# Optimization experiments

Hardware: AMD Instinct MI355X
Metric: run time of the kernel (lower is better)

## Reference

```python
import jax, jax.numpy as jnp
import numpy as np

L, B, T, C, H, D, F, W = 2, 2, 2048, 1024, 16, 64, 4096, 256
NEG = -1e9
EPS = 1e-6


def _rms(x, g):
    return x * jax.lax.rsqrt(jnp.mean(x * x, axis=-1, keepdims=True) + EPS) * g


def setup_inputs() -> dict:
    key = jax.random.key(0)
    ks = jax.random.split(key, 12)
    s = 0.02
    return {
        "x": jax.random.normal(ks[0], (B, T, C), jnp.float32),
        "retrieval_context": jax.random.normal(ks[1], (B, C), jnp.float32),
        "norm1_g": jnp.ones((L, C), jnp.float32),
        "Wqkv": jax.random.normal(ks[2], (L, C, 3 * C), jnp.float32) * s,
        "Wproj": jax.random.normal(ks[3], (L, C, C), jnp.float32) * s,
        "gate_W": jax.random.normal(ks[4], (L, C, 3), jnp.float32) * 0.01,
        "gate_b": jnp.zeros((L, 3), jnp.float32),
        "ret_W": jax.random.normal(ks[5], (L, C, C), jnp.float32) * 0.01,
        "norm2_g": jnp.ones((L, C), jnp.float32),
        "ffn_gate_W": jax.random.normal(ks[6], (L, C, F), jnp.float32) * s,
        "ffn_up_W": jax.random.normal(ks[7], (L, C, F), jnp.float32) * s,
        "ffn_down_W": jax.random.normal(ks[8], (L, F, C), jnp.float32) * s,
    }


def reference(x, retrieval_context, norm1_g, Wqkv, Wproj, gate_W, gate_b, ret_W,
              norm2_g, ffn_gate_W, ffn_up_W, ffn_down_W):
    # Sliding-window causal mask: key j visible to query i iff i-W+1 <= j <= i
    pos = jnp.arange(T)
    allowed = (pos[None, :] <= pos[:, None]) & (pos[None, :] >= pos[:, None] - W + 1)
    mask = jnp.where(allowed, 0.0, NEG).astype(x.dtype)  # (T, T)
    scale = 1.0 / np.sqrt(D)

    for l in range(L):
        h = _rms(x, norm1_g[l])                              # (B,T,C)
        qkv = h @ Wqkv[l]                                    # (B,T,3C)
        q, k, v = jnp.split(qkv, 3, axis=-1)
        q = q.reshape(B, T, H, D).transpose(0, 2, 1, 3)       # (B,H,T,D)
        k = k.reshape(B, T, H, D).transpose(0, 2, 1, 3)
        v = v.reshape(B, T, H, D).transpose(0, 2, 1, 3)
        scores = jnp.einsum("bhqd,bhkd->bhqk", q, k) * scale + mask
        attn = jax.nn.softmax(scores, axis=-1)
        o = jnp.einsum("bhqk,bhkd->bhqd", attn, v)
        attn_out = o.transpose(0, 2, 1, 3).reshape(B, T, C) @ Wproj[l]

        # TRN disabled: trn_out == 0, gate channel 1 pinned to -1e9
        gate_logits = h @ gate_W[l] + gate_b[l]               # (B,T,3)
        gate_logits = gate_logits.at[..., 1].set(NEG)
        gates = jax.nn.softmax(gate_logits, axis=-1)

        ret_out = (retrieval_context @ ret_W[l])[:, None, :]   # (B,1,C) broadcast over T
        mixed = gates[..., 0:1] * attn_out + gates[..., 2:3] * ret_out
        x = x + mixed

        h2 = _rms(x, norm2_g[l])
        ffn = (jax.nn.silu(h2 @ ffn_gate_W[l]) * (h2 @ ffn_up_W[l])) @ ffn_down_W[l]
        x = x + ffn
    return x
```

## Files before the change

### kernel.cpp

```cpp
#include <hip/hip_runtime.h>

#define L_ 2
#define B_ 2
#define T_ 2048
#define C_ 1024
#define H_ 16
#define D_ 64
#define F_ 4096
#define NTOK 4096
#define NELEM 4194304

typedef unsigned short u16;
typedef __attribute__((ext_vector_type(8))) short short8;
typedef __attribute__((ext_vector_type(4))) float float4v;

__device__ __forceinline__ float bf2f(u16 u) {
  unsigned v = ((unsigned)u) << 16;
  return __builtin_bit_cast(float, v);
}
__device__ __forceinline__ u16 f2bf(float f) {
  unsigned u = __builtin_bit_cast(unsigned, f);
  u += 0x7FFFu + ((u >> 16) & 1u);
  return (u16)(u >> 16);
}

__device__ __forceinline__ void xcd_swz(int& bx, int& by) {
  const int gy4 = gridDim.y >> 2;
  const int f = by * 16 + bx;
  const int k = f & 7, s = f >> 3;
  bx = ((k & 1) << 3) + (s & 7);
  by = (k >> 1) * gy4 + (s >> 3);
}

__global__ void k_copyf_acc(const float* __restrict__ in, float* __restrict__ out) {
  const int i = blockIdx.x * 256 + threadIdx.x;
  out[i] = in[i] + out[i];
}

__device__ __forceinline__ void rms_gate_tail(float* vloc, const float* __restrict__ g,
                                              u16* __restrict__ orow,
                                              const float* __restrict__ gw3,
                                              const float* __restrict__ gb3,
                                              float* __restrict__ gates, int row) {
  float s = vloc[0] * vloc[0] + vloc[1] * vloc[1] + vloc[2] * vloc[2] + vloc[3] * vloc[3];
#pragma unroll
  for (int o = 32; o; o >>= 1) s += __shfl_down(s, o);
  __shared__ float red[4];
  __shared__ float rsv;
  if ((threadIdx.x & 63) == 0) red[threadIdx.x >> 6] = s;
  __syncthreads();
  if (threadIdx.x == 0) {
    float t = red[0] + red[1] + red[2] + red[3];
    rsv = rsqrtf(t * (1.f / C_) + 1e-6f);
  }
  __syncthreads();
  const float rr = rsv;
  float s0 = 0.f, s2 = 0.f;
#pragma unroll
  for (int i = 0; i < 4; i++) {
    const int c = threadIdx.x + i * 256;
    const float h = vloc[i] * rr * g[c];
    orow[c] = f2bf(h);
    s0 += h * gw3[c * 3 + 0];
    s2 += h * gw3[c * 3 + 2];
  }
#pragma unroll
  for (int o = 32; o; o >>= 1) { s0 += __shfl_down(s0, o); s2 += __shfl_down(s2, o); }
  __shared__ float r0[4], r2[4];
  if ((threadIdx.x & 63) == 0) { r0[threadIdx.x >> 6] = s0; r2[threadIdx.x >> 6] = s2; }
  __syncthreads();
  if (threadIdx.x == 0) {
    const float l0 = r0[0] + r0[1] + r0[2] + r0[3] + gb3[0];
    const float l2 = r2[0] + r2[1] + r2[2] + r2[3] + gb3[2];
    const float m = fmaxf(l0, l2);
    const float e0 = __expf(l0 - m), e2 = __expf(l2 - m);
    const float inv = 1.f / (e0 + e2);
    gates[row * 2 + 0] = e0 * inv;
    gates[row * 2 + 1] = e2 * inv;
  }
}

__global__ __launch_bounds__(256) void k_rms_first(const float* __restrict__ xin,
                                                   const float* __restrict__ g,
                                                   float* __restrict__ x,
                                                   u16* __restrict__ out,
                                                   const float* __restrict__ gw3,
                                                   const float* __restrict__ gb3,
                                                   float* __restrict__ gates) {
  const int row = blockIdx.x;
  const float* sr = xin + (size_t)row * C_;
  float* xr = x + (size_t)row * C_;
  float vloc[4];
#pragma unroll
  for (int i = 0; i < 4; i++) {
    const int c = threadIdx.x + i * 256;
    const float v = sr[c];
    vloc[i] = v;
    xr[c] = v;
  }
  rms_gate_tail(vloc, g, out + (size_t)row * C_, gw3, gb3, gates, row);
}

__global__ __launch_bounds__(256) void k_rms_acc(float* __restrict__ x,
                                                 const float* __restrict__ pf,
                                                 const float* __restrict__ g,
                                                 u16* __restrict__ out,
                                                 const float* __restrict__ gw3,
                                                 const float* __restrict__ gb3,
                                                 float* __restrict__ gates) {
  const int row = blockIdx.x;
  float* xr = x + (size_t)row * C_;
  const float* pr = pf + (size_t)row * C_;
  float vloc[4];
#pragma unroll
  for (int i = 0; i < 4; i++) {
    const int c = threadIdx.x + i * 256;
    const float v = xr[c] + pr[c];
    vloc[i] = v;
    xr[c] = v;
  }
  rms_gate_tail(vloc, g, out + (size_t)row * C_, gw3, gb3, gates, row);
}

__global__ __launch_bounds__(256) void k_rms2mix(float* __restrict__ x,
                                                 const float* __restrict__ gates,
                                                 const float* __restrict__ ret,
                                                 const float* __restrict__ pf,
                                                 const float* __restrict__ g,
                                                 u16* __restrict__ out) {
  const int row = blockIdx.x;
  const int b = row >> 11;
  const float g2 = gates[row * 2 + 1];
  const float* rr_ = ret + b * C_;
  const float* pr = pf + (size_t)row * C_;
  float* xr = x + (size_t)row * C_;
  float vloc[4];
#pragma unroll
  for (int i = 0; i < 4; i++) {
    const int c = threadIdx.x + i * 256;
    const float v = xr[c] + pr[c] + g2 * rr_[c];
    vloc[i] = v;
    xr[c] = v;
  }
  float s = vloc[0] * vloc[0] + vloc[1] * vloc[1] + vloc[2] * vloc[2] + vloc[3] * vloc[3];
#pragma unroll
  for (int o = 32; o; o >>= 1) s += __shfl_down(s, o);
  __shared__ float red[4];
  __shared__ float rsv;
  if ((threadIdx.x & 63) == 0) red[threadIdx.x >> 6] = s;
  __syncthreads();
  if (threadIdx.x == 0) {
    float t = red[0] + red[1] + red[2] + red[3];
    rsv = rsqrtf(t * (1.f / C_) + 1e-6f);
  }
  __syncthreads();
  const float rr = rsv;
  u16* orow = out + (size_t)row * C_;
#pragma unroll
  for (int i = 0; i < 4; i++) {
    const int c = threadIdx.x + i * 256;
    orow[c] = f2bf(vloc[i] * rr * g[c]);
  }
}

__global__ void k_tr2(const float* __restrict__ s0, u16* __restrict__ d0,
                      int K0, int N0, int t0,
                      const float* __restrict__ s1, u16* __restrict__ d1,
                      int K1, int N1) {
  __shared__ float tile[32][33];
  int t = blockIdx.x;
  const float* src; u16* dst; int K, N;
  if (t < t0) { src = s0; dst = d0; K = K0; N = N0; }
  else { t -= t0; src = s1; dst = d1; K = K1; N = N1; }
  const int ntx = N >> 5;
  const int tx = t % ntx, ty = t / ntx;
  const int x = tx * 32 + threadIdx.x;
  const int y0 = ty * 32 + threadIdx.y;
#pragma unroll
  for (int i = 0; i < 32; i += 8) tile[threadIdx.y + i][threadIdx.x] = src[(size_t)(y0 + i) * N + x];
  __syncthreads();
  const int x2 = ty * 32 + threadIdx.x;
  const int y2 = tx * 32 + threadIdx.y;
#pragma unroll
  for (int i = 0; i < 32; i += 8) dst[(size_t)(y2 + i) * K + x2] = f2bf(tile[threadIdx.x][threadIdx.y + i]);
}

__global__ void k_tr1(const float* __restrict__ in, u16* __restrict__ out, int K, int N) {
  __shared__ float tile[32][33];
  const int ntx = N >> 5;
  const int tx = blockIdx.x % ntx, ty = blockIdx.x / ntx;
  const int x = tx * 32 + threadIdx.x;
  const int y0 = ty * 32 + threadIdx.y;
#pragma unroll
  for (int i = 0; i < 32; i += 8) tile[threadIdx.y + i][threadIdx.x] = in[(size_t)(y0 + i) * N + x];
  __syncthreads();
  const int x2 = ty * 32 + threadIdx.x;
  const int y2 = tx * 32 + threadIdx.y;
#pragma unroll
  for (int i = 0; i < 32; i += 8) out[(size_t)(y2 + i) * K + x2] = f2bf(tile[threadIdx.x][threadIdx.y + i]);
}

__global__ void k_vt(const u16* __restrict__ qkv, u16* __restrict__ Vt) {
  __shared__ u16 tile[32][34];
  const int jt = blockIdx.x;
  const int dt = blockIdx.y;
  const int bh = blockIdx.z;
  const int b = bh >> 4;
  const int h = bh & 15;
  const int tx = threadIdx.x, ty = threadIdx.y;
#pragma unroll
  for (int i = 0; i < 32; i += 8) {
    const int j = jt * 32 + ty + i;
    const int d = dt * 32 + tx;
    tile[ty + i][tx] = qkv[(size_t)(b * T_ + j) * (3 * C_) + 2 * C_ + h * D_ + d];
  }
  __syncthreads();
#pragma unroll
  for (int i = 0; i < 32; i += 8) {
    const int d = dt * 32 + ty + i;
    const int j = jt * 32 + tx;
    Vt[(size_t)(bh * D_ + d) * T_ + j] = tile[tx][ty + i];
  }
}

#define VMW(n) asm volatile("s_waitcnt vmcnt(" #n ")" ::: "memory")
#define LGKM0 asm volatile("s_waitcnt lgkmcnt(0)" ::: "memory")
#define GBAR() __builtin_amdgcn_s_barrier()
#define PRIO1() __builtin_amdgcn_s_setprio(1)
#define PRIO0() __builtin_amdgcn_s_setprio(0)

#define STG8(gsrc, grow0, dstbyte, kk)                                                    \
  do {                                                                                    \
    const u16* g0_ = (gsrc) + (size_t)((grow0) + wid * 8 + srow) * K + (kk) + scol;       \
    __builtin_amdgcn_global_load_lds(                                                     \
        (const __attribute__((address_space(1))) void*)g0_,                               \
        (__attribute__((address_space(3))) void*)(lc + (dstbyte) + wid * 8 * 128),        \
        16, 0, 0);                                                                        \
    const u16* g1_ = g0_ + (size_t)64 * K;                                                \
    __builtin_amdgcn_global_load_lds(                                                     \
        (const __attribute__((address_space(1))) void*)g1_,                               \
        (__attribute__((address_space(3))) void*)(lc + (dstbyte) + (64 + wid * 8) * 128), \
        16, 0, 0);                                                                        \
  } while (0)

#define RDA4(dst, bufbyte, ig0)                                                           \
  { _Pragma("unroll") for (int i_ = 0; i_ < 4; ++i_) {                                    \
      _Pragma("unroll") for (int s_ = 0; s_ < 2; ++s_)                                    \
        dst[i_][s_] = *(const short8*)(lc + (bufbyte) +                                   \
            (wm * 128 + ((ig0) + i_) * 16 + m16) * 128 + (((s_ * 4 + quad) ^ csw) * 16)); } }

#define RDB4(dst, bufbyte, jg0)                                                           \
  { _Pragma("unroll") for (int j_ = 0; j_ < 2; ++j_) {                                    \
      _Pragma("unroll") for (int s_ = 0; s_ < 2; ++s_)                                    \
        dst[j_][s_] = *(const short8*)(lc + (bufbyte) +                                   \
            (wn * 64 + ((jg0) + j_) * 16 + m16) * 128 + (((s_ * 4 + quad) ^ csw) * 16)); } }

#define RDBS(dst, bufbyte)                                                                \
  { _Pragma("unroll") for (int j_ = 0; j_ < 2; ++j_) {                                    \
      _Pragma("unroll") for (int s_ = 0; s_ < 2; ++s_)                                    \
        dst[j_][s_] = *(const short8*)(lc + (bufbyte) +                                   \
            (wn * 32 + j_ * 16 + m16) * 128 + (((s_ * 4 + quad) ^ csw) * 16)); } }

#define MM16(ig0, jg0, bv_)                                                               \
  { _Pragma("unroll") for (int i_ = 0; i_ < 4; ++i_) {                                    \
      _Pragma("unroll") for (int j_ = 0; j_ < 2; ++j_) {                                  \
        _Pragma("unroll") for (int s_ = 0; s_ < 2; ++s_)                                  \
          acc[(ig0) + i_][(jg0) + j_] = __builtin_amdgcn_mfma_f32_16x16x32_bf16(          \
              av[i_][s_], bv_[j_][s_], acc[(ig0) + i_][(jg0) + j_], 0, 0, 0); } } }

#define MMS(accv, ig0, bv_)                                                               \
  { _Pragma("unroll") for (int i_ = 0; i_ < 4; ++i_) {                                    \
      _Pragma("unroll") for (int j_ = 0; j_ < 2; ++j_) {                                  \
        _Pragma("unroll") for (int s_ = 0; s_ < 2; ++s_)                                  \
          accv[(ig0) + i_][j_] = __builtin_amdgcn_mfma_f32_16x16x32_bf16(                 \
              av[i_][s_], bv_[j_][s_], accv[(ig0) + i_][j_], 0, 0, 0); } } }

#define MMN(ig0, bv_)                                                                     \
  { _Pragma("unroll") for (int i_ = 0; i_ < 4; ++i_) {                                    \
      _Pragma("unroll") for (int j_ = 0; j_ < 2; ++j_) {                                  \
        _Pragma("unroll") for (int s_ = 0; s_ < 2; ++s_)                                  \
          acc[(ig0) + i_][j_] = __builtin_amdgcn_mfma_f32_16x16x32_bf16(                  \
              av8[(ig0) + i_][s_], bv_[j_][s_], acc[(ig0) + i_][j_], 0, 0, 0); } } }

__global__ __launch_bounds__(512, 2) void k_g256(const u16* __restrict__ A,
                                                 const u16* __restrict__ Bt,
                                                 u16* __restrict__ Cc,
                                                 int N, int K) {
  extern __shared__ __align__(16) u16 lds[];
  char* const lc = (char*)lds;
  enum { A0B = 0, B0B = 32768, A1B = 65536, B1B = 98304 };
  const int tid = threadIdx.x;
  const int wid = tid >> 6, lane = tid & 63;
  const int wm = wid >> 2, wn = wid & 3;
  const int quad = lane >> 4, m16 = lane & 15;
  const int srow = lane >> 3, sc = lane & 7;
  const int scol = ((sc ^ srow) & 7) * 8;
  const int csw = m16 & 7;
  int bx = blockIdx.x, by = blockIdx.y;
  xcd_swz(bx, by);
  const int m0 = bx * 256, n0 = by * 256;
  const int kbeg = 0;
  const int ntile = K >> 6;
  const int nit = ntile >> 1;

  float4v acc[8][4];
#pragma unroll
  for (int i = 0; i < 8; i++)
#pragma unroll
    for (int j = 0; j < 4; j++) acc[i][j] = (float4v){0.f, 0.f, 0.f, 0.f};
  short8 av[4][2], b01[2][2], b23[2][2];

  STG8(Bt, n0, B0B, kbeg);
  STG8(Bt, n0 + 128, B0B + 16384, kbeg);
  STG8(A, m0, A0B, kbeg);
  STG8(A, m0 + 128, A0B + 16384, kbeg);
  STG8(Bt, n0, B1B, kbeg + 64);
  STG8(Bt, n0 + 128, B1B + 16384, kbeg + 64);
  VMW(4);
  GBAR();

#pragma unroll 1
  for (int it = 0; it < nit; ++it) {
    const int t2 = 2 * it + 2, t3 = 2 * it + 3;
    const int k1 = kbeg + (2 * it + 1) * 64;
    const int k2 = kbeg + (t2 < ntile ? t2 : t2 - ntile) * 64;
    const int k3 = kbeg + (t3 < ntile ? t3 : t3 - ntile) * 64;
    RDA4(av, A0B, 0);
    RDB4(b01, B0B, 0);
    STG8(A, m0, A1B, k1);
    GBAR(); LGKM0;
    PRIO1(); MM16(0, 0, b01); PRIO0();
    GBAR();
    RDB4(b23, B0B, 2);
    STG8(A, m0 + 128, A1B + 16384, k1);
    GBAR(); LGKM0;
    PRIO1(); MM16(0, 2, b23); PRIO0();
    GBAR();
    RDA4(av, A0B, 4);
    STG8(Bt, n0, B0B, k2);
    GBAR(); LGKM0;
    PRIO1(); MM16(4, 2, b23); PRIO0();
    GBAR();
    STG8(Bt, n0 + 128, B0B + 16384, k2);
    VMW(4);
    GBAR(); LGKM0;
    PRIO1(); MM16(4, 0, b01); PRIO0();
    GBAR();
    RDA4(av, A1B, 0);
    RDB4(b01, B1B, 0);
    STG8(A, m0, A0B, k2);
    GBAR(); LGKM0;
    PRIO1(); MM16(0, 0, b01); PRIO0();
    GBAR();
    RDB4(b23, B1B, 2);
    STG8(A, m0 + 128, A0B + 16384, k2);
    GBAR(); LGKM0;
    PRIO1(); MM16(0, 2, b23); PRIO0();
    GBAR();
    RDA4(av, A1B, 4);
    STG8(Bt, n0, B1B, k3);
    GBAR(); LGKM0;
    PRIO1(); MM16(4, 2, b23); PRIO0();
    GBAR();
    STG8(Bt, n0 + 128, B1B + 16384, k3);
    VMW(4);
    GBAR(); LGKM0;
    PRIO1(); MM16(4, 0, b01); PRIO0();
    GBAR();
  }

#pragma unroll
  for (int i = 0; i < 8; i++) {
    const int row0 = m0 + wm * 128 + i * 16 + quad * 4;
#pragma unroll
    for (int j = 0; j < 4; j++) {
      const int col = n0 + wn * 64 + j * 16 + m16;
#pragma unroll
      for (int r = 0; r < 4; r++)
        Cc[(size_t)(row0 + r) * N + col] = f2bf(acc[i][j][r]);
    }
  }
}

template <int EPI>
__global__ __launch_bounds__(512, 2) void k_g256n(const u16* __restrict__ A,
                                                  const u16* __restrict__ Bt,
                                                  float* __restrict__ Xf,
                                                  float* __restrict__ Pf,
                                                  const float* __restrict__ gates,
                                                  int N, int K) {
  extern __shared__ __align__(16) u16 lds[];
  char* const lc = (char*)lds;
  enum { SA0 = 0, SB0 = 32768, SA1 = 49152, SB1 = 81920 };
  const int tid = threadIdx.x;
  const int wid = tid >> 6, lane = tid & 63;
  const int wm = wid >> 2, wn = wid & 3;
  const int quad = lane >> 4, m16 = lane & 15;
  const int srow = lane >> 3, sc = lane & 7;
  const int scol = ((sc ^ srow) & 7) * 8;
  const int csw = m16 & 7;
  int bx = blockIdx.x, by = blockIdx.y;
  xcd_swz(bx, by);
  const int m0 = bx * 256, n0 = by * 128;
  const int Kslice = K / gridDim.z;
  const int kbeg = blockIdx.z * Kslice;
  const int ntile = Kslice >> 6;
  const int nit = ntile >> 1;

  float4v acc[8][2];
#pragma unroll
  for (int i = 0; i < 8; i++)
#pragma unroll
    for (int j = 0; j < 2; j++) acc[i][j] = (float4v){0.f, 0.f, 0.f, 0.f};
  short8 av8[8][2], bv[2][2];

  STG8(Bt, n0, SB0, kbeg);
  STG8(A, m0, SA0, kbeg);
  STG8(A, m0 + 128, SA0 + 16384, kbeg);
  STG8(Bt, n0, SB1, kbeg + 64);
  STG8(A, m0, SA1, kbeg + 64);
  STG8(A, m0 + 128, SA1 + 16384, kbeg + 64);
  VMW(6);
  GBAR();

#pragma unroll 1
  for (int it = 0; it < nit; ++it) {
    const int t2 = 2 * it + 2, t3 = 2 * it + 3;
    const int k2 = kbeg + (t2 < ntile ? t2 : t2 - ntile) * 64;
    const int k3 = kbeg + (t3 < ntile ? t3 : t3 - ntile) * 64;
    RDA4(av8, SA0, 0);
    RDA4((&av8[4]), SA0, 4);
    RDBS(bv, SB0);
    GBAR(); LGKM0;
    PRIO1(); MMN(0, bv); PRIO0();
    GBAR();
    STG8(Bt, n0, SB0, k2);
    STG8(A, m0, SA0, k2);
    STG8(A, m0 + 128, SA0 + 16384, k2);
    VMW(6);
    GBAR(); LGKM0;
    PRIO1(); MMN(4, bv); PRIO0();
    GBAR();
    RDA4(av8, SA1, 0);
    RDA4((&av8[4]), SA1, 4);
    RDBS(bv, SB1);
    GBAR(); LGKM0;
    PRIO1(); MMN(0, bv); PRIO0();
    GBAR();
    STG8(Bt, n0, SB1, k3);
    STG8(A, m0, SA1, k3);
    STG8(A, m0 + 128, SA1 + 16384, k3);
    VMW(6);
    GBAR(); LGKM0;
    PRIO1(); MMN(4, bv); PRIO0();
    GBAR();
  }

#pragma unroll
  for (int i = 0; i < 8; i++) {
    const int row0 = m0 + wm * 128 + i * 16 + quad * 4;
#pragma unroll
    for (int j = 0; j < 2; j++) {
      const int col = n0 + wn * 32 + j * 16 + m16;
#pragma unroll
      for (int r = 0; r < 4; r++) {
        const size_t idx = (size_t)(row0 + r) * N + col;
        const float v = acc[i][j][r];
        const float sv = (EPI == 1) ? gates[(row0 + r) * 2] * v : v;
        if (blockIdx.z == 0) Pf[idx] = sv;
        else Xf[idx] += sv;
      }
    }
  }
}

__global__ __launch_bounds__(512, 2) void k_g256s(const u16* __restrict__ A,
                                                  const u16* __restrict__ Btg,
                                                  const u16* __restrict__ Btu,
                                                  u16* __restrict__ Cc,
                                                  int N, int K) {
  extern __shared__ __align__(16) u16 lds[];
  char* const lc = (char*)lds;
  enum { SA0 = 0, SG0 = 32768, SU0 = 49152, SA1 = 65536, SG1 = 98304, SU1 = 114688 };
  const int tid = threadIdx.x;
  const int wid = tid >> 6, lane = tid & 63;
  const int wm = wid >> 2, wn = wid & 3;
  const int quad = lane >> 4, m16 = lane & 15;
  const int srow = lane >> 3, sc = lane & 7;
  const int scol = ((sc ^ srow) & 7) * 8;
  const int csw = m16 & 7;
  int bx = blockIdx.x, by = blockIdx.y;
  xcd_swz(bx, by);
  const int m0 = bx * 256, n0 = by * 128;
  const int kbeg = 0;
  const int ntile = K >> 6;
  const int nit = ntile >> 1;

  float4v accg[8][2], accu[8][2];
#pragma unroll
  for (int i = 0; i < 8; i++)
#pragma unroll
    for (int j = 0; j < 2; j++) {
      accg[i][j] = (float4v){0.f, 0.f, 0.f, 0.f};
      accu[i][j] = (float4v){0.f, 0.f, 0.f, 0.f};
    }
  short8 av[4][2], bg[2][2], bu[2][2];

  STG8(Btg, n0, SG0, kbeg);
  STG8(Btu, n0, SU0, kbeg);
  STG8(A, m0, SA0, kbeg);
  STG8(A, m0 + 128, SA0 + 16384, kbeg);
  STG8(Btg, n0, SG1, kbeg + 64);
  STG8(Btu, n0, SU1, kbeg + 64);
  STG8(A, m0, SA1, kbeg + 64);
  VMW(6);
  GBAR();

#pragma unroll 1
  for (int it = 0; it < nit; ++it) {
    const int t2 = 2 * it + 2, t3 = 2 * it + 3;
    const int k1 = kbeg + (2 * it + 1) * 64;
    const int k2 = kbeg + (t2 < ntile ? t2 : t2 - ntile) * 64;
    const int k3 = kbeg + (t3 < ntile ? t3 : t3 - ntile) * 64;
    RDA4(av, SA0, 0);
    RDBS(bg, SG0);
    STG8(A, m0 + 128, SA1 + 16384, k1);
    GBAR(); LGKM0;
    PRIO1(); MMS(accg, 0, bg); PRIO0();
    GBAR();
    RDBS(bu, SU0);
    STG8(Btg, n0, SG0, k2);
    GBAR(); LGKM0;
    PRIO1(); MMS(accu, 0, bu); PRIO0();
    GBAR();
    RDA4(av, SA0, 4);
    STG8(Btu, n0, SU0, k2);
    GBAR(); LGKM0;
    PRIO1(); MMS(accu, 4, bu); PRIO0();
    GBAR();
    STG8(A, m0, SA0, k2);
    VMW(6);
    GBAR(); LGKM0;
    PRIO1(); MMS(accg, 4, bg); PRIO0();
    GBAR();
    RDA4(av, SA1, 0);
    RDBS(bg, SG1);
    STG8(A, m0 + 128, SA0 + 16384, k2);
    GBAR(); LGKM0;
    PRIO1(); MMS(accg, 0, bg); PRIO0();
    GBAR();
    RDBS(bu, SU1);
    STG8(Btg, n0, SG1, k3);
    GBAR(); LGKM0;
    PRIO1(); MMS(accu, 0, bu); PRIO0();
    GBAR();
    RDA4(av, SA1, 4);
    STG8(Btu, n0, SU1, k3);
    GBAR(); LGKM0;
    PRIO1(); MMS(accu, 4, bu); PRIO0();
    GBAR();
    STG8(A, m0, SA1, k3);
    VMW(6);
    GBAR(); LGKM0;
    PRIO1(); MMS(accg, 4, bg); PRIO0();
    GBAR();
  }

#pragma unroll
  for (int i = 0; i < 8; i++) {
    const int row0 = m0 + wm * 128 + i * 16 + quad * 4;
#pragma unroll
    for (int j = 0; j < 2; j++) {
      const int col = n0 + wn * 32 + j * 16 + m16;
#pragma unroll
      for (int r = 0; r < 4; r++) {
        const float g = accg[i][j][r];
        const float u = accu[i][j][r];
        Cc[(size_t)(row0 + r) * N + col] = f2bf(u * g / (1.f + __expf(-g)));
      }
    }
  }
}

__global__ __launch_bounds__(256) void k_attn(const u16* __restrict__ qkv,
                                              const u16* __restrict__ Vt,
                                              u16* __restrict__ o) {
  __shared__ u16 lds[4][16][290];
  const int wave = threadIdx.x >> 6;
  const int bid = ((blockIdx.x & 7) << 7) + (blockIdx.x >> 3);
  const int widG = bid * 4 + wave;
  const int lane = threadIdx.x & 63;
  const int quad = lane >> 4;
  const int c16 = lane & 15;
  const int qt = (widG & 127) * 16;
  const int h = (widG >> 7) & 15;
  const int b = widG >> 11;
  const size_t rs = 3 * C_;
  const int jt0 = qt - 256;

  const u16* qrow = qkv + (size_t)(b * T_ + qt + c16) * rs + h * D_ + quad * 8;
  const short8 a0 = *(const short8*)(qrow);
  const short8 a1 = *(const short8*)(qrow + 32);
  float4v S[17];
  const short8 z8 = (short8){0, 0, 0, 0, 0, 0, 0, 0};
#pragma unroll
  for (int t = 0; t < 17; t++) {
    if (jt0 + t * 16 + 15 < 0) { S[t] = (float4v){0.f, 0.f, 0.f, 0.f}; continue; }
    const int j = jt0 + t * 16 + c16;
    short8 b0 = z8, b1 = z8;
    if (j >= 0) {
      const u16* krow = qkv + (size_t)(b * T_ + j) * rs + C_ + h * D_ + quad * 8;
      b0 = *(const short8*)(krow);
      b1 = *(const short8*)(krow + 32);
    }
    float4v z = (float4v){0.f, 0.f, 0.f, 0.f};
    PRIO1();
    z = __builtin_amdgcn_mfma_f32_16x16x32_bf16(a0, b0, z, 0, 0, 0);
    z = __builtin_amdgcn_mfma_f32_16x16x32_bf16(a1, b1, z, 0, 0, 0);
    PRIO0();
    S[t] = z;
  }
#pragma unroll
  for (int r = 0; r < 4; r++) {
    const int q = qt + quad * 4 + r;
    float mx = -1.0e30f;
#pragma unroll
    for (int t = 0; t < 17; t++) {
      const int j = jt0 + t * 16 + c16;
      const int w = j - q + 255;
      const bool vis = (j >= 0) && (w >= 0) && (w < 256);
      if (vis) {
        const float s = S[t][r] * 0.125f;
        S[t][r] = s;
        mx = fmaxf(mx, s);
      } else {
        S[t][r] = -1.0e30f;
      }
    }
#pragma unroll
    for (int o2 = 1; o2 < 16; o2 <<= 1) mx = fmaxf(mx, __shfl_xor(mx, o2));
    float sum = 0.f;
#pragma unroll
    for (int t = 0; t < 17; t++) {
      const float e = (S[t][r] > -0.9e30f) ? __expf(S[t][r] - mx) : 0.f;
      S[t][r] = e;
      sum += e;
    }
#pragma unroll
    for (int o2 = 1; o2 < 16; o2 <<= 1) sum += __shfl_xor(sum, o2);
    const float inv = 1.f / fmaxf(sum, 1e-30f);
    const int prow = quad * 4 + r;
#pragma unroll
    for (int t = 0; t < 17; t++) lds[wave][prow][t * 16 + c16] = f2bf(S[t][r] * inv);
    lds[wave][prow][272 + c16] = 0;
  }
  __syncthreads();

  float4v acc[4];
#pragma unroll
  for (int md = 0; md < 4; md++) acc[md] = (float4v){0.f, 0.f, 0.f, 0.f};
  const u16* vtb = Vt + (size_t)((b * H_ + h) * D_) * T_;
  const uint* prow32 = (const uint*)(&lds[wave][c16][0]);
  union { short8 s8; uint u[4]; } bf;
#pragma unroll
  for (int c = 0; c < 9; c++) {
    const int jbase = jt0 + c * 32;
    if (jbase + 31 < 0) continue;
#pragma unroll
    for (int w2 = 0; w2 < 4; w2++) bf.u[w2] = prow32[c * 16 + quad * 4 + w2];
    int j0 = jbase + quad * 8;
    j0 = (j0 < 0) ? 0 : ((j0 > T_ - 8) ? (T_ - 8) : j0);
    PRIO1();
#pragma unroll
    for (int md = 0; md < 4; md++) {
      const short8 af = *(const short8*)(vtb + (size_t)(md * 16 + c16) * T_ + j0);
      acc[md] = __builtin_amdgcn_mfma_f32_16x16x32_bf16(af, bf.s8, acc[md], 0, 0, 0);
    }
    PRIO0();
  }
#pragma unroll
  for (int md = 0; md < 4; md++) {
    uint u0 = (uint)f2bf(acc[md][0]) | ((uint)f2bf(acc[md][1]) << 16);
    uint u1 = (uint)f2bf(acc[md][2]) | ((uint)f2bf(acc[md][3]) << 16);
    uint2 pk = make_uint2(u0, u1);
    u16* dst = o + (size_t)(b * T_ + qt + c16) * C_ + h * D_ + md * 16 + quad * 4;
    *(uint2*)dst = pk;
  }
}

__global__ void k_ret2(const float* __restrict__ rc, const float* __restrict__ rW,
                       float* __restrict__ ret) {
  const int l = blockIdx.x >> 3;
  const int bid = blockIdx.x & 7;
  const int b = bid >> 2;
  const int col = (bid & 3) * 256 + threadIdx.x;
  const float* rWl = rW + (size_t)l * C_ * C_;
  float s = 0.f;
  for (int k = 0; k < C_; k++) s += rc[b * C_ + k] * rWl[(size_t)k * C_ + col];
  ret[(size_t)l * B_ * C_ + b * C_ + col] = s;
}

extern "C" void kernel_launch(void* const* d_in, const int* in_sizes, int n_in,
                              void* d_out, int out_size, void* d_ws, size_t ws_size,
                              hipStream_t stream) {
  (void)in_sizes; (void)n_in; (void)out_size; (void)ws_size;
  const float* xin  = (const float*)d_in[0];
  const float* rc   = (const float*)d_in[1];
  const float* n1g  = (const float*)d_in[2];
  const float* Wqkv = (const float*)d_in[3];
  const float* Wpro = (const float*)d_in[4];
  const float* gW   = (const float*)d_in[5];
  const float* gb   = (const float*)d_in[6];
  const float* rW   = (const float*)d_in[7];
  const float* n2g  = (const float*)d_in[8];
  const float* fgW  = (const float*)d_in[9];
  const float* fuW  = (const float*)d_in[10];
  const float* fdW  = (const float*)d_in[11];

  static bool attr_done = false;
  if (!attr_done) {
    hipFuncSetAttribute((const void*)k_g256, hipFuncAttributeMaxDynamicSharedMemorySize, 131072);
    hipFuncSetAttribute((const void*)k_g256s, hipFuncAttributeMaxDynamicSharedMemorySize, 131072);
    hipFuncSetAttribute((const void*)k_g256n<1>, hipFuncAttributeMaxDynamicSharedMemorySize, 98304);
    hipFuncSetAttribute((const void*)k_g256n<2>, hipFuncAttributeMaxDynamicSharedMemorySize, 98304);
    attr_done = true;
  }

  char* w = (char*)d_ws;
  float* gates = (float*)(w);
  float* retb  = (float*)(w + 32768);
  float* xf32  = (float*)(w + 65536);
  u16* hbuf    = (u16*)(w + 65536 + (size_t)NELEM * 4);
  u16* big     = hbuf + NELEM;
  u16* qkv  = big;
  u16* obuf = big + (size_t)NTOK * 3 * C_;
  u16* gbuf = big;
  u16* wT  = (u16*)d_out;
  u16* wTp = wT + (size_t)3 * C_ * C_;
  u16* Vt  = (u16*)d_out + (size_t)NELEM;
  u16* wT2 = Vt;
  float* Pf  = (float*)d_out;
  float* Pf2 = (float*)big;

  k_ret2<<<16, 256, 0, stream>>>(rc, rW, retb);

  for (int l = 0; l < L_; l++) {
    if (l == 0)
      k_rms_first<<<NTOK, 256, 0, stream>>>(xin, n1g, xf32, hbuf,
                                            gW, gb, gates);
    else
      k_rms_acc<<<NTOK, 256, 0, stream>>>(xf32, Pf, n1g + l * C_, hbuf,
                                          gW + (size_t)l * C_ * 3, gb + l * 3, gates);
    k_tr2<<<3072 + 1024, dim3(32, 8), 0, stream>>>(
        Wqkv + (size_t)l * C_ * 3 * C_, wT, C_, 3 * C_, 3072,
        Wpro + (size_t)l * C_ * C_, wTp, C_, C_);
    k_g256<<<dim3(NTOK / 256, 3 * C_ / 256, 1), 512, 131072, stream>>>(
        hbuf, wT, qkv, 3 * C_, C_);
    k_vt<<<dim3(64, 2, 32), dim3(32, 8), 0, stream>>>(qkv, Vt);
    k_attn<<<1024, 256, 0, stream>>>(qkv, Vt, obuf);
    k_g256n<1><<<dim3(NTOK / 256, C_ / 128, 2), 512, 98304, stream>>>(
        obuf, wTp, xf32, Pf2, gates, C_, C_);
    k_rms2mix<<<NTOK, 256, 0, stream>>>(xf32, gates, retb + (size_t)l * B_ * C_,
                                        Pf2, n2g + l * C_, hbuf);
    k_tr2<<<4096 + 4096, dim3(32, 8), 0, stream>>>(
        fgW + (size_t)l * C_ * F_, wT, C_, F_, 4096,
        fuW + (size_t)l * C_ * F_, wT2, C_, F_);
    k_g256s<<<dim3(NTOK / 256, F_ / 128, 1), 512, 131072, stream>>>(
        hbuf, wT, wT2, gbuf, F_, C_);
    k_tr1<<<4096, dim3(32, 8), 0, stream>>>(fdW + (size_t)l * F_ * C_, hbuf, F_, C_);
    k_g256n<2><<<dim3(NTOK / 256, C_ / 128, 2), 512, 98304, stream>>>(
        gbuf, hbuf, xf32, Pf, nullptr, C_, F_);
  }

  k_copyf_acc<<<NELEM / 256, 256, 0, stream>>>(xf32, (float*)d_out);
}
```

Measured before the change: 786.5 us.

## Fuse V-transpose into QKV GEMM epilogue and unify SwiGLU GEMM via interleaved weights

The QKV GEMM epilogue now writes the V columns directly in transposed (b,h,d,t) layout, which removes the separate k_vt transpose kernel. The FFN gate and up weights are transposed into one interleaved matrix (16-row groups alternating gate/up), so the generic 256x256 GEMM computes both and applies SiLU*up in its epilogue, replacing the specialised k_g256s kernel. The retrieval projection kernel is also re-split across 256 blocks with a shared-memory K reduction for more parallelism. The trade-off is strided 8-byte Vt stores in the epilogue and a branch per column group.

New measurement: 746.2 us. 5.1% less time.

```diff
diff --git a/kernel.cpp b/kernel.cpp
--- a/kernel.cpp
+++ b/kernel.cpp
@@ -185,6 +185,31 @@
   for (int i = 0; i < 32; i += 8) dst[(size_t)(y2 + i) * K + x2] = f2bf(tile[threadIdx.x][threadIdx.y + i]);
 }
 
+__global__ void k_tr2i(const float* __restrict__ s0, const float* __restrict__ s1,
+                       u16* __restrict__ dst, int t0) {
+  __shared__ float tile[32][33];
+  int t = blockIdx.x;
+  const float* src; int ofs;
+  if (t < t0) { src = s0; ofs = 0; }
+  else { t -= t0; src = s1; ofs = 16; }
+  const int N = F_, K = C_;
+  const int ntx = N >> 5;
+  const int tx = t % ntx, ty = t / ntx;
+  const int x = tx * 32 + threadIdx.x;
+  const int y0 = ty * 32 + threadIdx.y;
+#pragma unroll
+  for (int i = 0; i < 32; i += 8) tile[threadIdx.y + i][threadIdx.x] = src[(size_t)(y0 + i) * N + x];
+  __syncthreads();
+  const int x2 = ty * 32 + threadIdx.x;
+  const int y2 = tx * 32 + threadIdx.y;
+#pragma unroll
+  for (int i = 0; i < 32; i += 8) {
+    const int n = y2 + i;
+    const int rowp = ((n >> 4) << 5) + (n & 15) + ofs;
+    dst[(size_t)rowp * K + x2] = f2bf(tile[threadIdx.x][threadIdx.y + i]);
+  }
+}
+
 __global__ void k_tr1(const float* __restrict__ in, u16* __restrict__ out, int K, int N) {
   __shared__ float tile[32][33];
   const int ntx = N >> 5;
@@ -198,29 +223,6 @@
   const int y2 = tx * 32 + threadIdx.y;
 #pragma unroll
   for (int i = 0; i < 32; i += 8) out[(size_t)(y2 + i) * K + x2] = f2bf(tile[threadIdx.x][threadIdx.y + i]);
-}
-
-__global__ void k_vt(const u16* __restrict__ qkv, u16* __restrict__ Vt) {
-  __shared__ u16 tile[32][34];
-  const int jt = blockIdx.x;
-  const int dt = blockIdx.y;
-  const int bh = blockIdx.z;
-  const int b = bh >> 4;
-  const int h = bh & 15;
-  const int tx = threadIdx.x, ty = threadIdx.y;
-#pragma unroll
-  for (int i = 0; i < 32; i += 8) {
-    const int j = jt * 32 + ty + i;
-    const int d = dt * 32 + tx;
-    tile[ty + i][tx] = qkv[(size_t)(b * T_ + j) * (3 * C_) + 2 * C_ + h * D_ + d];
-  }
-  __syncthreads();
-#pragma unroll
-  for (int i = 0; i < 32; i += 8) {
-    const int d = dt * 32 + ty + i;
-    const int j = jt * 32 + tx;
-    Vt[(size_t)(bh * D_ + d) * T_ + j] = tile[tx][ty + i];
-  }
 }
 
 #define VMW(n) asm volatile("s_waitcnt vmcnt(" #n ")" ::: "memory")
@@ -268,13 +270,6 @@
           acc[(ig0) + i_][(jg0) + j_] = __builtin_amdgcn_mfma_f32_16x16x32_bf16(          \
               av[i_][s_], bv_[j_][s_], acc[(ig0) + i_][(jg0) + j_], 0, 0, 0); } } }
 
-#define MMS(accv, ig0, bv_)                                                               \
-  { _Pragma("unroll") for (int i_ = 0; i_ < 4; ++i_) {                                    \
-      _Pragma("unroll") for (int j_ = 0; j_ < 2; ++j_) {                                  \
-        _Pragma("unroll") for (int s_ = 0; s_ < 2; ++s_)                                  \
-          accv[(ig0) + i_][j_] = __builtin_amdgcn_mfma_f32_16x16x32_bf16(                 \
-              av[i_][s_], bv_[j_][s_], accv[(ig0) + i_][j_], 0, 0, 0); } } }
-
 #define MMN(ig0, bv_)                                                                     \
   { _Pragma("unroll") for (int i_ = 0; i_ < 4; ++i_) {                                    \
       _Pragma("unroll") for (int j_ = 0; j_ < 2; ++j_) {                                  \
@@ -282,9 +277,11 @@
           acc[(ig0) + i_][j_] = __builtin_amdgcn_mfma_f32_16x16x32_bf16(                  \
               av8[(ig0) + i_][s_], bv_[j_][s_], acc[(ig0) + i_][j_], 0, 0, 0); } } }
 
+template <int EPI>
 __global__ __launch_bounds__(512, 2) void k_g256(const u16* __restrict__ A,
                                                  const u16* __restrict__ Bt,
                                                  u16* __restrict__ Cc,
+                                                 u16* __restrict__ Vt,
                                                  int N, int K) {
   extern __shared__ __align__(16) u16 lds[];
   char* const lc = (char*)lds;
@@ -369,15 +366,44 @@
     GBAR();
   }
 
-#pragma unroll
-  for (int i = 0; i < 8; i++) {
-    const int row0 = m0 + wm * 128 + i * 16 + quad * 4;
-#pragma unroll
-    for (int j = 0; j < 4; j++) {
-      const int col = n0 + wn * 64 + j * 16 + m16;
-#pragma unroll
-      for (int r = 0; r < 4; r++)
-        Cc[(size_t)(row0 + r) * N + col] = f2bf(acc[i][j][r]);
+  if (EPI == 3) {
+#pragma unroll
+    for (int i = 0; i < 8; i++) {
+      const int row0 = m0 + wm * 128 + i * 16 + quad * 4;
+#pragma unroll
+      for (int jp = 0; jp < 2; jp++) {
+        const int col = by * 128 + wn * 32 + jp * 16 + m16;
+#pragma unroll
+        for (int r = 0; r < 4; r++) {
+          const float g = acc[i][jp * 2][r];
+          const float u = acc[i][jp * 2 + 1][r];
+          Cc[(size_t)(row0 + r) * N + col] = f2bf(u * g / (1.f + __expf(-g)));
+        }
+      }
+    }
+  } else {
+#pragma unroll
+    for (int i = 0; i < 8; i++) {
+      const int row0 = m0 + wm * 128 + i * 16 + quad * 4;
+#pragma unroll
+      for (int j = 0; j < 4; j++) {
+        const int colb = n0 + wn * 64 + j * 16;
+        if (colb >= 2 * C_) {
+          const int d = colb + m16 - 2 * C_;
+          const int bh = d >> 6;
+          const int dd = d & 63;
+          const int b_ = row0 >> 11;
+          const int tok = row0 & (T_ - 1);
+          uint u0 = (uint)f2bf(acc[i][j][0]) | ((uint)f2bf(acc[i][j][1]) << 16);
+          uint u1 = (uint)f2bf(acc[i][j][2]) | ((uint)f2bf(acc[i][j][3]) << 16);
+          *(uint2*)(Vt + (size_t)((b_ * H_ + bh) * D_ + dd) * T_ + tok) = make_uint2(u0, u1);
+        } else {
+          const int col = colb + m16;
+#pragma unroll
+          for (int r = 0; r < 4; r++)
+            Cc[(size_t)(row0 + r) * N + col] = f2bf(acc[i][j][r]);
+        }
+      }
     }
   }
 }
@@ -474,114 +500,6 @@
   }
 }
 
-__global__ __launch_bounds__(512, 2) void k_g256s(const u16* __restrict__ A,
-                                                  const u16* __restrict__ Btg,
-                                                  const u16* __restrict__ Btu,
-                                                  u16* __restrict__ Cc,
-                                                  int N, int K) {
-  extern __shared__ __align__(16) u16 lds[];
-  char* const lc = (char*)lds;
-  enum { SA0 = 0, SG0 = 32768, SU0 = 49152, SA1 = 65536, SG1 = 98304, SU1 = 114688 };
-  const int tid = threadIdx.x;
-  const int wid = tid >> 6, lane = tid & 63;
-  const int wm = wid >> 2, wn = wid & 3;
-  const int quad = lane >> 4, m16 = lane & 15;
-  const int srow = lane >> 3, sc = lane & 7;
-  const int scol = ((sc ^ srow) & 7) * 8;
-  const int csw = m16 & 7;
-  int bx = blockIdx.x, by = blockIdx.y;
-  xcd_swz(bx, by);
-  const int m0 = bx * 256, n0 = by * 128;
-  const int kbeg = 0;
-  const int ntile = K >> 6;
-  const int nit = ntile >> 1;
-
-  float4v accg[8][2], accu[8][2];
-#pragma unroll
-  for (int i = 0; i < 8; i++)
-#pragma unroll
-    for (int j = 0; j < 2; j++) {
-      accg[i][j] = (float4v){0.f, 0.f, 0.f, 0.f};
-      accu[i][j] = (float4v){0.f, 0.f, 0.f, 0.f};
-    }
-  short8 av[4][2], bg[2][2], bu[2][2];
-
-  STG8(Btg, n0, SG0, kbeg);
-  STG8(Btu, n0, SU0, kbeg);
-  STG8(A, m0, SA0, kbeg);
-  STG8(A, m0 + 128, SA0 + 16384, kbeg);
-  STG8(Btg, n0, SG1, kbeg + 64);
-  STG8(Btu, n0, SU1, kbeg + 64);
-  STG8(A, m0, SA1, kbeg + 64);
-  VMW(6);
-  GBAR();
-
-#pragma unroll 1
-  for (int it = 0; it < nit; ++it) {
-    const int t2 = 2 * it + 2, t3 = 2 * it + 3;
-    const int k1 = kbeg + (2 * it + 1) * 64;
-    const int k2 = kbeg + (t2 < ntile ? t2 : t2 - ntile) * 64;
-    const int k3 = kbeg + (t3 < ntile ? t3 : t3 - ntile) * 64;
-    RDA4(av, SA0, 0);
-    RDBS(bg, SG0);
-    STG8(A, m0 + 128, SA1 + 16384, k1);
-    GBAR(); LGKM0;
-    PRIO1(); MMS(accg, 0, bg); PRIO0();
-    GBAR();
-    RDBS(bu, SU0);
-    STG8(Btg, n0, SG0, k2);
-    GBAR(); LGKM0;
-    PRIO1(); MMS(accu, 0, bu); PRIO0();
-    GBAR();
-    RDA4(av, SA0, 4);
-    STG8(Btu, n0, SU0, k2);
-    GBAR(); LGKM0;
-    PRIO1(); MMS(accu, 4, bu); PRIO0();
-    GBAR();
-    STG8(A, m0, SA0, k2);
-    VMW(6);
-    GBAR(); LGKM0;
-    PRIO1(); MMS(accg, 4, bg); PRIO0();
-    GBAR();
-    RDA4(av, SA1, 0);
-    RDBS(bg, SG1);
-    STG8(A, m0 + 128, SA0 + 16384, k2);
-    GBAR(); LGKM0;
-    PRIO1(); MMS(accg, 0, bg); PRIO0();
-    GBAR();
-    RDBS(bu, SU1);
-    STG8(Btg, n0, SG1, k3);
-    GBAR(); LGKM0;
-    PRIO1(); MMS(accu, 0, bu); PRIO0();
-    GBAR();
-    RDA4(av, SA1, 4);
-    STG8(Btu, n0, SU1, k3);
-    GBAR(); LGKM0;
-    PRIO1(); MMS(accu, 4, bu); PRIO0();
-    GBAR();
-    STG8(A, m0, SA1, k3);
-    VMW(6);
-    GBAR(); LGKM0;
-    PRIO1(); MMS(accg, 4, bg); PRIO0();
-    GBAR();
-  }
-
-#pragma unroll
-  for (int i = 0; i < 8; i++) {
-    const int row0 = m0 + wm * 128 + i * 16 + quad * 4;
-#pragma unroll
-    for (int j = 0; j < 2; j++) {
-      const int col = n0 + wn * 32 + j * 16 + m16;
-#pragma unroll
-      for (int r = 0; r < 4; r++) {
-        const float g = accg[i][j][r];
-        const float u = accu[i][j][r];
-        Cc[(size_t)(row0 + r) * N + col] = f2bf(u * g / (1.f + __expf(-g)));
-      }
-    }
-  }
-}
-
 __global__ __launch_bounds__(256) void k_attn(const u16* __restrict__ qkv,
                                               const u16* __restrict__ Vt,
                                               u16* __restrict__ o) {
@@ -688,16 +606,27 @@
   }
 }
 
-__global__ void k_ret2(const float* __restrict__ rc, const float* __restrict__ rW,
-                       float* __restrict__ ret) {
-  const int l = blockIdx.x >> 3;
-  const int bid = blockIdx.x & 7;
-  const int b = bid >> 2;
-  const int col = (bid & 3) * 256 + threadIdx.x;
+__global__ __launch_bounds__(256) void k_ret2(const float* __restrict__ rc,
+                                              const float* __restrict__ rW,
+                                              float* __restrict__ ret) {
+  const int l = blockIdx.x >> 7;
+  const int b = (blockIdx.x >> 6) & 1;
+  const int cc = blockIdx.x & 63;
+  const int col = cc * 16 + (threadIdx.x & 15);
+  const int ks = threadIdx.x >> 4;
   const float* rWl = rW + (size_t)l * C_ * C_;
+  const float* rcb = rc + b * C_;
   float s = 0.f;
-  for (int k = 0; k < C_; k++) s += rc[b * C_ + k] * rWl[(size_t)k * C_ + col];
-  ret[(size_t)l * B_ * C_ + b * C_ + col] = s;
+  for (int k = ks * 64; k < ks * 64 + 64; k++) s += rcb[k] * rWl[(size_t)k * C_ + col];
+  __shared__ float red[256];
+  red[threadIdx.x] = s;
+  __syncthreads();
+  if (threadIdx.x < 16) {
+    float t = 0.f;
+#pragma unroll
+    for (int i = 0; i < 16; i++) t += red[i * 16 + threadIdx.x];
+    ret[(size_t)l * B_ * C_ + b * C_ + cc * 16 + threadIdx.x] = t;
+  }
 }
 
 extern "C" void kernel_launch(void* const* d_in, const int* in_sizes, int n_in,
@@ -719,8 +648,8 @@
 
   static bool attr_done = false;
   if (!attr_done) {
-    hipFuncSetAttribute((const void*)k_g256, hipFuncAttributeMaxDynamicSharedMemorySize, 131072);
-    hipFuncSetAttribute((const void*)k_g256s, hipFuncAttributeMaxDynamicSharedMemorySize, 131072);
+    hipFuncSetAttribute((const void*)k_g256<0>, hipFuncAttributeMaxDynamicSharedMemorySize, 131072);
+    hipFuncSetAttribute((const void*)k_g256<3>, hipFuncAttributeMaxDynamicSharedMemorySize, 131072);
     hipFuncSetAttribute((const void*)k_g256n<1>, hipFuncAttributeMaxDynamicSharedMemorySize, 98304);
     hipFuncSetAttribute((const void*)k_g256n<2>, hipFuncAttributeMaxDynamicSharedMemorySize, 98304);
     attr_done = true;
@@ -738,11 +667,11 @@
   u16* wT  = (u16*)d_out;
   u16* wTp = wT + (size_t)3 * C_ * C_;
   u16* Vt  = (u16*)d_out + (size_t)NELEM;
-  u16* wT2 = Vt;
+  u16* Bcat = (u16*)d_out;
   float* Pf  = (float*)d_out;
   float* Pf2 = (float*)big;
 
-  k_ret2<<<16, 256, 0, stream>>>(rc, rW, retb);
+  k_ret2<<<256, 256, 0, stream>>>(rc, rW, retb);
 
   for (int l = 0; l < L_; l++) {
     if (l == 0)
@@ -754,19 +683,17 @@
     k_tr2<<<3072 + 1024, dim3(32, 8), 0, stream>>>(
         Wqkv + (size_t)l * C_ * 3 * C_, wT, C_, 3 * C_, 3072,
         Wpro + (size_t)l * C_ * C_, wTp, C_, C_);
-    k_g256<<<dim3(NTOK / 256, 3 * C_ / 256, 1), 512, 131072, stream>>>(
-        hbuf, wT, qkv, 3 * C_, C_);
-    k_vt<<<dim3(64, 2, 32), dim3(32, 8), 0, stream>>>(qkv, Vt);
+    k_g256<0><<<dim3(NTOK / 256, 3 * C_ / 256, 1), 512, 131072, stream>>>(
+        hbuf, wT, qkv, Vt, 3 * C_, C_);
     k_attn<<<1024, 256, 0, stream>>>(qkv, Vt, obuf);
     k_g256n<1><<<dim3(NTOK / 256, C_ / 128, 2), 512, 98304, stream>>>(
         obuf, wTp, xf32, Pf2, gates, C_, C_);
     k_rms2mix<<<NTOK, 256, 0, stream>>>(xf32, gates, retb + (size_t)l * B_ * C_,
                                         Pf2, n2g + l * C_, hbuf);
-    k_tr2<<<4096 + 4096, dim3(32, 8), 0, stream>>>(
-        fgW + (size_t)l * C_ * F_, wT, C_, F_, 4096,
-        fuW + (size_t)l * C_ * F_, wT2, C_, F_);
-    k_g256s<<<dim3(NTOK / 256, F_ / 128, 1), 512, 131072, stream>>>(
-        hbuf, wT, wT2, gbuf, F_, C_);
+    k_tr2i<<<4096 + 4096, dim3(32, 8), 0, stream>>>(
+        fgW + (size_t)l * C_ * F_, fuW + (size_t)l * C_ * F_, Bcat, 4096);
+    k_g256<3><<<dim3(NTOK / 256, 2 * F_ / 256, 1), 512, 131072, stream>>>(
+        hbuf, Bcat, gbuf, nullptr, F_, C_);
     k_tr1<<<4096, dim3(32, 8), 0, stream>>>(fdW + (size_t)l * F_ * C_, hbuf, F_, C_);
     k_g256n<2><<<dim3(NTOK / 256, C_ / 128, 2), 512, 98304, stream>>>(
         gbuf, hbuf, xf32, Pf, nullptr, C_, F_);
```
